# Kernel optimization log

Hardware: AMD Instinct MI355X
Metric: run time of the kernel (lower is better)

## Reference

```python
import jax, jax.numpy as jnp
import numpy as np

C = 16      # internal_channel
DG = 8      # deform groups
KK = 9      # 3x3 kernel


def conv2d(x, w, b, pad):
    out = jax.lax.conv_general_dilated(
        x, w, (1, 1), [(pad, pad), (pad, pad)],
        dimension_numbers=('NCHW', 'OIHW', 'NCHW'))
    return out + b[None, :, None, None]


def feature_extraction(img, w1, b1, w2, b2, w3, b3):
    f1 = jax.nn.relu(conv2d(img, w1, b1, 1))   # [B,C,H,W]
    f2 = jax.nn.relu(conv2d(f1, w2, b2, 0))    # [B,C,H-2,W-2]
    f3 = jax.nn.relu(conv2d(f2, w3, b3, 0))    # [B,C,H-4,W-4]
    return [f1, f2, f3]


def deform_conv(x, offset, w, b):
    # x: [B,C,H,W]; offset: [B, DG*KK*2, H, W] (y,x pairs); w: [Cout,C,3,3]
    B, Cin, H, W = x.shape
    Cg = Cin // DG
    off = offset.reshape(B, DG, KK, 2, H, W)
    ky = jnp.repeat(jnp.arange(3) - 1, 3)  # kernel y offsets (pad=1)
    kx = jnp.tile(jnp.arange(3) - 1, 3)
    base_y = jnp.arange(H).reshape(1, 1, 1, H, 1)
    base_x = jnp.arange(W).reshape(1, 1, 1, 1, W)
    sy = base_y + ky.reshape(1, 1, KK, 1, 1) + off[:, :, :, 0]  # [B,DG,KK,H,W]
    sx = base_x + kx.reshape(1, 1, KK, 1, 1) + off[:, :, :, 1]
    y0 = jnp.floor(sy)
    x0 = jnp.floor(sx)
    wy = (sy - y0)[:, :, None]  # [B,DG,1,KK,H,W]
    wx = (sx - x0)[:, :, None]
    y0i = y0.astype(jnp.int32)
    x0i = x0.astype(jnp.int32)
    xg = x.reshape(B, DG, Cg, H * W)

    def gather(yy, xx):
        valid = (yy >= 0) & (yy < H) & (xx >= 0) & (xx < W)  # zero pad outside
        idx = (jnp.clip(yy, 0, H - 1) * W + jnp.clip(xx, 0, W - 1))
        idx_b = jnp.broadcast_to(idx.reshape(B, DG, 1, KK, H * W), (B, DG, Cg, KK, H * W))
        src = jnp.broadcast_to(xg[:, :, :, None, :], (B, DG, Cg, KK, H * W))
        g = jnp.take_along_axis(src, idx_b, axis=-1).reshape(B, DG, Cg, KK, H, W)
        return g * valid[:, :, None].astype(x.dtype)

    v00 = gather(y0i, x0i)
    v01 = gather(y0i, x0i + 1)
    v10 = gather(y0i + 1, x0i)
    v11 = gather(y0i + 1, x0i + 1)
    s = (v00 * (1 - wy) * (1 - wx) + v01 * (1 - wy) * wx
         + v10 * wy * (1 - wx) + v11 * wy * wx)
    s = s.reshape(B, Cin, KK, H, W)
    out = jnp.einsum('bckhw,ock->bohw', s, w.reshape(w.shape[0], Cin, KK))
    return out + b[None, :, None, None]


def setup_inputs() -> dict:
    key = jax.random.key(0)
    ks = jax.random.split(key, 24)
    B, H, W = 4, 192, 192
    sc = 0.05
    d = {
        'ref_image': jax.random.normal(ks[0], (B, C, H, W), jnp.float32),
        'unreg_image': jax.random.normal(ks[1], (B, C, H, W), jnp.float32),
        'fe_w1': jax.random.normal(ks[2], (C, C, 3, 3), jnp.float32) * sc,
        'fe_b1': jnp.zeros((C,), jnp.float32),
        'fe_w2': jax.random.normal(ks[3], (C, C, 3, 3), jnp.float32) * sc,
        'fe_b2': jnp.zeros((C,), jnp.float32),
        'fe_w3': jax.random.normal(ks[4], (C, C, 3, 3), jnp.float32) * sc,
        'fe_b3': jnp.zeros((C,), jnp.float32),
        'off_w0': jax.random.normal(ks[5], (C, 2 * C, 3, 3), jnp.float32) * sc,
        'off_b0': jnp.zeros((C,), jnp.float32),
        'off_w1': jax.random.normal(ks[6], (C, 2 * C, 3, 3), jnp.float32) * sc,
        'off_b1': jnp.zeros((C,), jnp.float32),
        'off_w2': jax.random.normal(ks[7], (C, 2 * C, 3, 3), jnp.float32) * sc,
        'off_b2': jnp.zeros((C,), jnp.float32),
        'dcn_off_w': jax.random.normal(ks[8], (2 * DG * KK, C, 3, 3), jnp.float32) * sc,
        'dcn_off_b': jnp.zeros((2 * DG * KK,), jnp.float32),
        'dcn_w': jax.random.normal(ks[9], (C, C, 3, 3), jnp.float32) * sc,
        'dcn_b': jnp.zeros((C,), jnp.float32),
    }
    return d


def reference(ref_image, unreg_image, fe_w1, fe_b1, fe_w2, fe_b2, fe_w3, fe_b3,
              off_w0, off_b0, off_w1, off_b1, off_w2, off_b2,
              dcn_off_w, dcn_off_b, dcn_w, dcn_b):
    ref_f = feature_extraction(ref_image, fe_w1, fe_b1, fe_w2, fe_b2, fe_w3, fe_b3)
    unr_f = feature_extraction(unreg_image, fe_w1, fe_b1, fe_w2, fe_b2, fe_w3, fe_b3)
    off_ws = [(off_w0, off_b0), (off_w1, off_b1), (off_w2, off_b2)]
    aligned = [None, None, None]
    for i in range(2, -1, -1):  # coarse-to-fine as in the source loop
        cat = jnp.concatenate([ref_f[i], unr_f[i]], axis=1)        # [B,2C,h,w]
        off_feat = jax.nn.relu(conv2d(cat, off_ws[i][0], off_ws[i][1], 1))
        offsets = conv2d(off_feat, dcn_off_w, dcn_off_b, 1)        # [B,2*DG*KK,h,w]
        aligned[i] = deform_conv(unr_f[i], offsets, dcn_w, dcn_b)
    return tuple(aligned)
```

## Files before the change

kernel.cpp:

```cpp
#include <hip/hip_runtime.h>

typedef unsigned int uint;
typedef unsigned short ushort;
typedef __attribute__((ext_vector_type(8))) short bf16x8;
typedef __attribute__((ext_vector_type(4))) float f32x4;

__device__ inline ushort f2bf(float f) {
    uint u = __float_as_uint(f);
    u += 0x7fff + ((u >> 16) & 1);
    return (ushort)(u >> 16);
}
__device__ inline uint pkbf(float lo, float hi) {
    uint r;
    asm("v_cvt_pk_bf16_f32 %0, %1, %2" : "=v"(r) : "v"(lo), "v"(hi));
    return r;
}
__device__ inline float bflo(uint w) { return __uint_as_float(w << 16); }
__device__ inline float bfhi(uint w) { return __uint_as_float(w & 0xffff0000u); }

__global__ void packall_k(
    const float* __restrict__ fe_w1, const float* __restrict__ fe_w2,
    const float* __restrict__ fe_w3, const float* __restrict__ off_w0,
    const float* __restrict__ off_w1, const float* __restrict__ off_w2,
    const float* __restrict__ dcn_off_w, const float* __restrict__ dcn_w,
    ushort* __restrict__ pf1, ushort* __restrict__ pf2, ushort* __restrict__ pf3,
    ushort* __restrict__ po0, ushort* __restrict__ po1, ushort* __restrict__ po2,
    ushort* __restrict__ pow_, ushort* __restrict__ pd) {
    const int y = blockIdx.y;
    int i = blockIdx.x * 256 + threadIdx.x;
    const float* w; ushort* pk; int CIN, NT, KS;
    switch (y) {
        case 0: w = fe_w1;  pk = pf1;  CIN = 16; NT = 1; KS = 5; break;
        case 1: w = fe_w2;  pk = pf2;  CIN = 16; NT = 1; KS = 5; break;
        case 2: w = fe_w3;  pk = pf3;  CIN = 16; NT = 1; KS = 5; break;
        case 3: w = off_w0; pk = po0;  CIN = 32; NT = 1; KS = 9; break;
        case 4: w = off_w1; pk = po1;  CIN = 32; NT = 1; KS = 9; break;
        case 5: w = off_w2; pk = po2;  CIN = 32; NT = 1; KS = 9; break;
        case 6: w = dcn_off_w; pk = pow_; CIN = 16; NT = 9; KS = 5; break;
        default: w = dcn_w; pk = pd;   CIN = 16; NT = 1; KS = 5; break;
    }
    if (i >= KS * NT * 512) return;
    int e = i & 7, lane = (i >> 3) & 63, rest = i >> 9;
    int nt = rest % NT, ks = rest / NT;
    int k = ks * 32 + (lane >> 4) * 8 + e;
    int n = nt * 16 + (lane & 15);
    int t, ci;
    if (CIN == 16) { t = k >> 4; ci = k & 15; } else { t = k >> 5; ci = k & 31; }
    float v = (t < 9) ? w[(n * CIN + ci) * 9 + t] : 0.f;
    pk[i] = f2bf(v);
}

template <bool PLANAR>
__launch_bounds__(256)
__global__ void fe_mfma_k(const float* __restrict__ pA, const float* __restrict__ pB,
                          const ushort* __restrict__ catin,
                          const ushort* __restrict__ pack, const float* __restrict__ bias,
                          ushort* __restrict__ catout,
                          int H, int W, int OH, int OW, int pad) {
    __shared__ ushort patch[324 * 16];
    const int tid = threadIdx.x;
    const int tx0 = blockIdx.x * 16, ty0 = blockIdx.y * 16;
    const int b = blockIdx.z & 3, img = blockIdx.z >> 2;
    const int bx = tx0 - pad, by = ty0 - pad;
    const int HW = H * W;

    if (PLANAR) {
        const float* inb = (img ? pB : pA) + (size_t)(b * 16) * HW;
        for (int pos = tid; pos < 324; pos += 256) {
            int r = pos / 18, c = pos - r * 18;
            int gy = by + r, gx = bx + c;
            bool ok = (unsigned)gy < (unsigned)H && (unsigned)gx < (unsigned)W;
            int base = gy * W + gx;
            uint o16[8];
#pragma unroll
            for (int ii = 0; ii < 8; ++ii) {
                float lo = ok ? inb[(2 * ii) * HW + base] : 0.f;
                float hi = ok ? inb[(2 * ii + 1) * HW + base] : 0.f;
                o16[ii] = (uint)f2bf(lo) | ((uint)f2bf(hi) << 16);
            }
            *(uint4*)(patch + pos * 16) = *(uint4*)&o16[0];
            *(uint4*)(patch + pos * 16 + 8) = *(uint4*)&o16[4];
        }
    } else {
        for (int c = tid; c < 648; c += 256) {
            int pos = c >> 1, h = c & 1;
            int r = pos / 18, col = pos - r * 18;
            int gy = by + r, gx = bx + col;
            uint4 v = make_uint4(0, 0, 0, 0);
            if ((unsigned)gy < (unsigned)H && (unsigned)gx < (unsigned)W)
                v = *(const uint4*)(catin + ((size_t)(b * H + gy) * W + gx) * 32 + img * 16 + h * 8);
            *(uint4*)(patch + pos * 16 + h * 8) = v;
        }
    }
    __syncthreads();

    const int lane = tid & 63, wv = tid >> 6;
    const int g = lane >> 4, ci0 = (g & 1) * 8, rowx = lane & 15;
    f32x4 acc[4];
    float bv = bias[rowx];
#pragma unroll
    for (int m = 0; m < 4; ++m) acc[m] = f32x4{bv, bv, bv, bv};

#pragma unroll
    for (int ks = 0; ks < 5; ++ks) {
        int t = 2 * ks + (g >> 1);
        int dy = t < 9 ? t / 3 : 0;
        int dx = t < 9 ? t - (t / 3) * 3 : 0;
        bf16x8 a[4];
#pragma unroll
        for (int m = 0; m < 4; ++m) {
            int r = wv * 4 + m + dy, cc = rowx + dx;
            a[m] = *(const bf16x8*)(patch + (r * 18 + cc) * 16 + ci0);
        }
        bf16x8 bfrag = *(const bf16x8*)((const uint4*)pack + ks * 64 + lane);
#pragma unroll
        for (int m = 0; m < 4; ++m)
            acc[m] = __builtin_amdgcn_mfma_f32_16x16x32_bf16(a[m], bfrag, acc[m], 0, 0, 0);
    }

    const int oxb = g * 4;
#pragma unroll
    for (int m = 0; m < 4; ++m) {
        int gy = ty0 + wv * 4 + m;
        if (gy >= OH) continue;
#pragma unroll
        for (int j = 0; j < 4; ++j) {
            int gx = tx0 + oxb + j;
            if (gx < OW)
                catout[((size_t)(b * OH + gy) * OW + gx) * 32 + img * 16 + rowx] =
                    f2bf(fmaxf(acc[m][j], 0.f));
        }
    }
}

__launch_bounds__(256)
__global__ void off_mfma_k(const ushort* __restrict__ c0, const ushort* __restrict__ c1,
                           const ushort* __restrict__ c2,
                           const ushort* __restrict__ pk0, const ushort* __restrict__ pk1,
                           const ushort* __restrict__ pk2,
                           const float* __restrict__ b0, const float* __restrict__ b1,
                           const float* __restrict__ b2,
                           ushort* __restrict__ f0, ushort* __restrict__ f1,
                           ushort* __restrict__ f2) {
    const int z = blockIdx.z, s = z >> 2, b = z & 3;
    const int H = 192 - 2 * s, W = H;
    const ushort* cat  = s == 0 ? c0 : (s == 1 ? c1 : c2);
    const ushort* pack = s == 0 ? pk0 : (s == 1 ? pk1 : pk2);
    const float* bias  = s == 0 ? b0 : (s == 1 ? b1 : b2);
    ushort* out        = s == 0 ? f0 : (s == 1 ? f1 : f2);

    __shared__ ushort patch[324 * 32];
    const int tid = threadIdx.x;
    const int tx0 = blockIdx.x * 16, ty0 = blockIdx.y * 16;
    const int bx = tx0 - 1, by = ty0 - 1;

    for (int c = tid; c < 1296; c += 256) {
        int pos = c >> 2, h = c & 3;
        int r = pos / 18, col = pos - r * 18;
        int gy = by + r, gx = bx + col;
        uint4 v = make_uint4(0, 0, 0, 0);
        if ((unsigned)gy < (unsigned)H && (unsigned)gx < (unsigned)W)
            v = *(const uint4*)(cat + ((size_t)(b * H + gy) * W + gx) * 32 + h * 8);
        *(uint4*)(patch + pos * 32 + h * 8) = v;
    }
    __syncthreads();

    const int lane = tid & 63, wv = tid >> 6;
    const int g = lane >> 4, ci0 = g * 8, rowx = lane & 15;
    f32x4 acc[4];
    float bv = bias[rowx];
#pragma unroll
    for (int m = 0; m < 4; ++m) acc[m] = f32x4{bv, bv, bv, bv};

#pragma unroll
    for (int ks = 0; ks < 9; ++ks) {
        int dy = ks / 3, dx = ks - (ks / 3) * 3;
        bf16x8 a[4];
#pragma unroll
        for (int m = 0; m < 4; ++m) {
            int r = wv * 4 + m + dy, cc = rowx + dx;
            a[m] = *(const bf16x8*)(patch + (r * 18 + cc) * 32 + ci0);
        }
        bf16x8 bfrag = *(const bf16x8*)((const uint4*)pack + ks * 64 + lane);
#pragma unroll
        for (int m = 0; m < 4; ++m)
            acc[m] = __builtin_amdgcn_mfma_f32_16x16x32_bf16(a[m], bfrag, acc[m], 0, 0, 0);
    }

    const int oxb = g * 4;
#pragma unroll
    for (int m = 0; m < 4; ++m) {
        int gy = ty0 + wv * 4 + m;
        if (gy >= H) continue;
#pragma unroll
        for (int j = 0; j < 4; ++j) {
            int gx = tx0 + oxb + j;
            if (gx < W)
                out[((size_t)(b * H + gy) * W + gx) * 16 + rowx] = f2bf(fmaxf(acc[m][j], 0.f));
        }
    }
}

__launch_bounds__(256)
__global__ void dcn_fused_k(const ushort* __restrict__ c0, const ushort* __restrict__ c1,
                            const ushort* __restrict__ c2,
                            const ushort* __restrict__ fb0, const ushort* __restrict__ fb1,
                            const ushort* __restrict__ fb2,
                            const ushort* __restrict__ owPack, const float* __restrict__ ob,
                            const ushort* __restrict__ pd, const float* __restrict__ db,
                            float* __restrict__ o0, float* __restrict__ o1,
                            float* __restrict__ o2) {
    const int z = blockIdx.z;
    const int s = z >> 2, b = z & 3;
    const int H = 192 - 2 * s, W = H;
    const ushort* cat = s == 0 ? c0 : (s == 1 ? c1 : c2);
    const ushort* fb  = s == 0 ? fb0 : (s == 1 ? fb1 : fb2);
    float* out        = s == 0 ? o0 : (s == 1 ? o1 : o2);
    const int HW = H * W;
    const size_t pixb = (size_t)b * HW;

    __shared__ uint   xtu[8 * 484];
    __shared__ ushort ot[4 * 16 * 152];

    const int tid = threadIdx.x;
    const int tx0 = blockIdx.x * 16, ty0 = blockIdx.y * 16;

    {
        const int bx3 = tx0 - 3, by3 = ty0 - 3;
        for (int pos = tid; pos < 484; pos += 256) {
            int r = pos / 22, c = pos - r * 22;
            int gy2 = by3 + r, gx2 = bx3 + c;
            uint4 va = make_uint4(0, 0, 0, 0), vb = va;
            if ((unsigned)gy2 < (unsigned)H && (unsigned)gx2 < (unsigned)W) {
                const ushort* src = cat + (pixb + gy2 * W + gx2) * 32 + 16;
                va = *(const uint4*)src;
                vb = *(const uint4*)(src + 8);
            }
            xtu[0 * 484 + pos] = va.x; xtu[1 * 484 + pos] = va.y;
            xtu[2 * 484 + pos] = va.z; xtu[3 * 484 + pos] = va.w;
            xtu[4 * 484 + pos] = vb.x; xtu[5 * 484 + pos] = vb.y;
            xtu[6 * 484 + pos] = vb.z; xtu[7 * 484 + pos] = vb.w;
        }
    }
    __syncthreads();

    const int lane = tid & 63, wv = tid >> 6;
    const int g = lane >> 4, rowx = lane & 15, half = g & 1;
    const int ci0 = half * 8;
    const int px = tx0 + rowx;
    const float bv2 = db[rowx];
    ushort* otw = ot + wv * (16 * 152);

#pragma unroll 1
    for (int m = 0; m < 4; ++m) {
        const int py = ty0 + wv * 4 + m;

        auto loadA = [&](int ks) -> uint4 {
            int t = 2 * ks + (g >> 1);
            int tc = t < 9 ? t : 0;
            int dy = tc / 3, dx = tc - (tc / 3) * 3;
            int gya = ty0 - 1 + wv * 4 + m + dy;
            int gxa = tx0 - 1 + rowx + dx;
            uint4 r = make_uint4(0, 0, 0, 0);
            if ((unsigned)gya < (unsigned)H && (unsigned)gxa < (unsigned)W)
                r = *(const uint4*)(fb + ((size_t)(b * H + gya) * W + gxa) * 16 + ci0);
            return r;
        };

        f32x4 acc[9];
#pragma unroll
        for (int n = 0; n < 9; ++n) {
            float bv = ob[n * 16 + rowx];
            acc[n] = f32x4{bv, bv, bv, bv};
        }
        uint4 avc = loadA(0);
#pragma unroll 1
        for (int ks = 0; ks < 5; ++ks) {
            uint4 avn = make_uint4(0, 0, 0, 0);
            if (ks < 4) avn = loadA(ks + 1);
            bf16x8 a = *(bf16x8*)&avc;
            const uint4* bp = (const uint4*)owPack + (size_t)(ks * 9) * 64 + lane;
#pragma unroll
            for (int n = 0; n < 9; ++n) {
                bf16x8 bfrag = *(const bf16x8*)(bp + (size_t)n * 64);
                acc[n] = __builtin_amdgcn_mfma_f32_16x16x32_bf16(a, bfrag, acc[n], 0, 0, 0);
            }
            avc = avn;
        }

#pragma unroll
        for (int n = 0; n < 9; ++n) {
            int ch = n * 16 + rowx;
            int dg = ch / 18;
            int rem = ch - dg * 18;
            int col = (rem >> 1) * 16 + dg * 2 + (rem & 1);
            uint p01 = pkbf(acc[n][0], acc[n][1]);
            uint p23 = pkbf(acc[n][2], acc[n][3]);
            otw[(g * 4 + 0) * 152 + col] = (ushort)p01;
            otw[(g * 4 + 1) * 152 + col] = (ushort)(p01 >> 16);
            otw[(g * 4 + 2) * 152 + col] = (ushort)p23;
            otw[(g * 4 + 3) * 152 + col] = (ushort)(p23 >> 16);
        }

        auto loadOV = [&](int ks) -> uint4 {
            int t = 2 * ks + (g >> 1);
            uint4 r = make_uint4(0, 0, 0, 0);
            if (t < 9) r = *(const uint4*)(otw + rowx * 152 + t * 16 + half * 8);
            return r;
        };

        f32x4 acc2 = f32x4{bv2, bv2, bv2, bv2};
        uint4 ovc = loadOV(0);
#pragma unroll 1
        for (int ks = 0; ks < 5; ++ks) {
            uint4 ovn = make_uint4(0, 0, 0, 0);
            if (ks < 4) ovn = loadOV(ks + 1);
            const int t = 2 * ks + (g >> 1);
            const bool tv = (t < 9);
            const int t3 = t / 3;
            const int ky = (tv ? t3 : 0) - 1, kx = (tv ? t - t3 * 3 : 0) - 1;

            uint a2[4];
            if (tv) {
                uint ovv[4] = {ovc.x, ovc.y, ovc.z, ovc.w};
#pragma unroll
                for (int d = 0; d < 4; ++d) {
                    const int dgA = half * 4 + d;
                    uint u = ovv[d];
                    float sy = (float)(py + ky) + bflo(u);
                    float sx = (float)(px + kx) + bfhi(u);
                    float fy = floorf(sy), fx = floorf(sx);
                    int y0 = (int)fy, x0 = (int)fx;
                    float wy = sy - fy, wx = sx - fx;
                    float wy1 = 1.f - wy, wx1 = 1.f - wx;
                    float w00 = wy1 * wx1, w01 = wy1 * wx, w10 = wy * wx1, w11 = wy * wx;
                    int ly = y0 - (ty0 - 3), lx = x0 - (tx0 - 3);
                    float2 v00, v01, v10, v11;
                    if ((unsigned)ly <= 20u && (unsigned)lx <= 20u) {
                        const uint* tt = &xtu[dgA * 484 + ly * 22 + lx];
                        uint u00 = tt[0], u01 = tt[1], u10 = tt[22], u11 = tt[23];
                        v00 = make_float2(bflo(u00), bfhi(u00));
                        v01 = make_float2(bflo(u01), bfhi(u01));
                        v10 = make_float2(bflo(u10), bfhi(u10));
                        v11 = make_float2(bflo(u11), bfhi(u11));
                    } else {
                        v00 = v01 = v10 = v11 = make_float2(0.f, 0.f);
                        bool y0v = (unsigned)y0 < (unsigned)H;
                        bool y1v = (unsigned)(y0 + 1) < (unsigned)H;
                        bool x0v = (unsigned)x0 < (unsigned)W;
                        bool x1v = (unsigned)(x0 + 1) < (unsigned)W;
                        const ushort* cg = cat + ((size_t)pixb + (size_t)y0 * W + x0) * 32 + 16 + 2 * dgA;
                        if (y0v && x0v) { uint uu = *(const uint*)cg;                 v00 = make_float2(bflo(uu), bfhi(uu)); }
                        if (y0v && x1v) { uint uu = *(const uint*)(cg + 32);          v01 = make_float2(bflo(uu), bfhi(uu)); }
                        if (y1v && x0v) { uint uu = *(const uint*)(cg + 32 * W);      v10 = make_float2(bflo(uu), bfhi(uu)); }
                        if (y1v && x1v) { uint uu = *(const uint*)(cg + 32 * W + 32); v11 = make_float2(bflo(uu), bfhi(uu)); }
                    }
                    float s0 = w00 * v00.x + w01 * v01.x + w10 * v10.x + w11 * v11.x;
                    float s1 = w00 * v00.y + w01 * v01.y + w10 * v10.y + w11 * v11.y;
                    a2[d] = pkbf(s0, s1);
                }
            } else {
                a2[0] = a2[1] = a2[2] = a2[3] = 0u;
            }
            uint4 av = make_uint4(a2[0], a2[1], a2[2], a2[3]);
            bf16x8 af = *(bf16x8*)&av;
            bf16x8 dfrag = *(const bf16x8*)((const uint4*)pd + ks * 64 + lane);
            acc2 = __builtin_amdgcn_mfma_f32_16x16x32_bf16(af, dfrag, acc2, 0, 0, 0);
            ovc = ovn;
        }

        if (py < H) {
            float* op = out + (size_t)(b * 16 + rowx) * HW + (size_t)py * W;
#pragma unroll
            for (int j = 0; j < 4; ++j) {
                int gx2 = tx0 + g * 4 + j;
                if (gx2 < W) op[gx2] = acc2[j];
            }
        }
    }
}

extern "C" void kernel_launch(void* const* d_in, const int* in_sizes, int n_in,
                              void* d_out, int out_size, void* d_ws, size_t ws_size,
                              hipStream_t stream) {
    const float* ref_image = (const float*)d_in[0];
    const float* unreg_image = (const float*)d_in[1];
    const float* fe_w1 = (const float*)d_in[2];
    const float* fe_b1 = (const float*)d_in[3];
    const float* fe_w2 = (const float*)d_in[4];
    const float* fe_b2 = (const float*)d_in[5];
    const float* fe_w3 = (const float*)d_in[6];
    const float* fe_b3 = (const float*)d_in[7];
    const float* off_w0 = (const float*)d_in[8];
    const float* off_b0 = (const float*)d_in[9];
    const float* off_w1 = (const float*)d_in[10];
    const float* off_b1 = (const float*)d_in[11];
    const float* off_w2 = (const float*)d_in[12];
    const float* off_b2 = (const float*)d_in[13];
    const float* dcn_off_w = (const float*)d_in[14];
    const float* dcn_off_b = (const float*)d_in[15];
    const float* dcn_w = (const float*)d_in[16];
    const float* dcn_b = (const float*)d_in[17];

    const size_t pix[3] = {4ul * 192 * 192, 4ul * 190 * 190, 4ul * 188 * 188};
    const size_t szf[3] = {pix[0] * 16, pix[1] * 16, pix[2] * 16};

    size_t o = 0;
    auto take = [&](size_t bytes) {
        void* r = (char*)d_ws + o;
        o += (bytes + 255) & ~(size_t)255;
        return r;
    };
    ushort* cat[3]; ushort* fb[3];
    ushort* pf[3]; ushort* po[3]; ushort* owPack; ushort* pd;
    for (int s = 0; s < 3; ++s) cat[s] = (ushort*)take(pix[s] * 32 * 2);
    for (int s = 0; s < 3; ++s) fb[s] = (ushort*)take(pix[s] * 16 * 2);
    for (int s = 0; s < 3; ++s) pf[s] = (ushort*)take(2560 * 2);
    for (int s = 0; s < 3; ++s) po[s] = (ushort*)take(4608 * 2);
    owPack = (ushort*)take(23040 * 2);
    pd = (ushort*)take(2560 * 2);

    float* out0 = (float*)d_out;
    float* out1 = out0 + szf[0];
    float* out2 = out1 + szf[1];

    dim3 blk(256);

    packall_k<<<dim3(90, 8), blk, 0, stream>>>(
        fe_w1, fe_w2, fe_w3, off_w0, off_w1, off_w2, dcn_off_w, dcn_w,
        pf[0], pf[1], pf[2], po[0], po[1], po[2], owPack, pd);

    fe_mfma_k<true><<<dim3(12, 12, 8), blk, 0, stream>>>(
        ref_image, unreg_image, nullptr, pf[0], fe_b1, cat[0], 192, 192, 192, 192, 1);
    fe_mfma_k<false><<<dim3(12, 12, 8), blk, 0, stream>>>(
        nullptr, nullptr, cat[0], pf[1], fe_b2, cat[1], 192, 192, 190, 190, 0);
    fe_mfma_k<false><<<dim3(12, 12, 8), blk, 0, stream>>>(
        nullptr, nullptr, cat[1], pf[2], fe_b3, cat[2], 190, 190, 188, 188, 0);

    off_mfma_k<<<dim3(12, 12, 12), blk, 0, stream>>>(
        cat[0], cat[1], cat[2], po[0], po[1], po[2],
        off_b0, off_b1, off_b2, fb[0], fb[1], fb[2]);

    dcn_fused_k<<<dim3(12, 12, 12), blk, 0, stream>>>(
        cat[0], cat[1], cat[2], fb[0], fb[1], fb[2],
        owPack, dcn_off_b, pd, dcn_b, out0, out1, out2);
}
```

Before: 174.4 us.

## Software-pipeline next row's offset-conv loads across the deformable sampling stage

The offset-conv operand loads and MFMA stage for row m+1 are moved so they overlap the bilinear sampling stage of row m. All five A fragments for the next row are issued before the sampling loop, and the next row's offset MFMAs and LDS repack run after the current row's output store. The first row is computed in a prologue. This hides global-load latency behind ALU and LDS work, at the cost of about 20 extra VGPRs for the prefetched operands. A small hoist also precomputes the float base coordinates per kernel tap.

```diff
diff --git a/kernel.cpp b/kernel.cpp
--- a/kernel.cpp
+++ b/kernel.cpp
@@ -251,43 +251,39 @@
     const float bv2 = db[rowx];
     ushort* otw = ot + wv * (16 * 152);
 
-#pragma unroll 1
-    for (int m = 0; m < 4; ++m) {
-        const int py = ty0 + wv * 4 + m;
-
-        auto loadA = [&](int ks) -> uint4 {
-            int t = 2 * ks + (g >> 1);
-            int tc = t < 9 ? t : 0;
-            int dy = tc / 3, dx = tc - (tc / 3) * 3;
-            int gya = ty0 - 1 + wv * 4 + m + dy;
-            int gxa = tx0 - 1 + rowx + dx;
-            uint4 r = make_uint4(0, 0, 0, 0);
-            if ((unsigned)gya < (unsigned)H && (unsigned)gxa < (unsigned)W)
-                r = *(const uint4*)(fb + ((size_t)(b * H + gya) * W + gxa) * 16 + ci0);
-            return r;
-        };
-
-        f32x4 acc[9];
+    auto loadA = [&](int ks, int mrow) -> uint4 {
+        int t = 2 * ks + (g >> 1);
+        int tc = t < 9 ? t : 0;
+        int dy = tc / 3, dx = tc - (tc / 3) * 3;
+        int gya = ty0 - 1 + wv * 4 + mrow + dy;
+        int gxa = tx0 - 1 + rowx + dx;
+        uint4 r = make_uint4(0, 0, 0, 0);
+        if ((unsigned)gya < (unsigned)H && (unsigned)gxa < (unsigned)W)
+            r = *(const uint4*)(fb + ((size_t)(b * H + gya) * W + gxa) * 16 + ci0);
+        return r;
+    };
+
+    auto mfma45 = [&](uint4 a0, uint4 a1, uint4 a2c, uint4 a3, uint4 a4,
+                      f32x4 (&acc)[9]) {
 #pragma unroll
         for (int n = 0; n < 9; ++n) {
             float bv = ob[n * 16 + rowx];
             acc[n] = f32x4{bv, bv, bv, bv};
         }
-        uint4 avc = loadA(0);
 #pragma unroll 1
         for (int ks = 0; ks < 5; ++ks) {
-            uint4 avn = make_uint4(0, 0, 0, 0);
-            if (ks < 4) avn = loadA(ks + 1);
-            bf16x8 a = *(bf16x8*)&avc;
+            uint4 avv = ks == 0 ? a0 : ks == 1 ? a1 : ks == 2 ? a2c : ks == 3 ? a3 : a4;
+            bf16x8 a = *(bf16x8*)&avv;
             const uint4* bp = (const uint4*)owPack + (size_t)(ks * 9) * 64 + lane;
 #pragma unroll
             for (int n = 0; n < 9; ++n) {
                 bf16x8 bfrag = *(const bf16x8*)(bp + (size_t)n * 64);
                 acc[n] = __builtin_amdgcn_mfma_f32_16x16x32_bf16(a, bfrag, acc[n], 0, 0, 0);
             }
-            avc = avn;
-        }
-
+        }
+    };
+
+    auto repack = [&](f32x4 (&acc)[9]) {
 #pragma unroll
         for (int n = 0; n < 9; ++n) {
             int ch = n * 16 + rowx;
@@ -301,6 +297,26 @@
             otw[(g * 4 + 2) * 152 + col] = (ushort)p23;
             otw[(g * 4 + 3) * 152 + col] = (ushort)(p23 >> 16);
         }
+    };
+
+    {
+        uint4 a0 = loadA(0, 0), a1 = loadA(1, 0), a2c = loadA(2, 0),
+              a3 = loadA(3, 0), a4 = loadA(4, 0);
+        f32x4 acc[9];
+        mfma45(a0, a1, a2c, a3, a4, acc);
+        repack(acc);
+    }
+
+#pragma unroll 1
+    for (int m = 0; m < 4; ++m) {
+        const int py = ty0 + wv * 4 + m;
+        const int mn = m + 1;
+
+        uint4 na0, na1, na2, na3, na4;
+        if (mn < 4) {
+            na0 = loadA(0, mn); na1 = loadA(1, mn); na2 = loadA(2, mn);
+            na3 = loadA(3, mn); na4 = loadA(4, mn);
+        }
 
         auto loadOV = [&](int ks) -> uint4 {
             int t = 2 * ks + (g >> 1);
@@ -318,7 +334,8 @@
             const int t = 2 * ks + (g >> 1);
             const bool tv = (t < 9);
             const int t3 = t / 3;
-            const int ky = (tv ? t3 : 0) - 1, kx = (tv ? t - t3 * 3 : 0) - 1;
+            const float pyk = (float)(py + (tv ? t3 : 0) - 1);
+            const float pxk = (float)(px + (tv ? t - t3 * 3 : 0) - 1);
 
             uint a2[4];
             if (tv) {
@@ -327,8 +344,8 @@
                 for (int d = 0; d < 4; ++d) {
                     const int dgA = half * 4 + d;
                     uint u = ovv[d];
-                    float sy = (float)(py + ky) + bflo(u);
-                    float sx = (float)(px + kx) + bfhi(u);
+                    float sy = pyk + bflo(u);
+                    float sx = pxk + bfhi(u);
                     float fy = floorf(sy), fx = floorf(sx);
                     int y0 = (int)fy, x0 = (int)fx;
                     float wy = sy - fy, wx = sx - fx;
@@ -349,7 +366,7 @@
                         bool y1v = (unsigned)(y0 + 1) < (unsigned)H;
                         bool x0v = (unsigned)x0 < (unsigned)W;
                         bool x1v = (unsigned)(x0 + 1) < (unsigned)W;
-                        const ushort* cg = cat + ((size_t)pixb + (size_t)y0 * W + x0) * 32 + 16 + 2 * dgA;
+                        const ushort* cg = cat + (pixb + (size_t)y0 * W + x0) * 32 + 16 + 2 * dgA;
                         if (y0v && x0v) { uint uu = *(const uint*)cg;                 v00 = make_float2(bflo(uu), bfhi(uu)); }
                         if (y0v && x1v) { uint uu = *(const uint*)(cg + 32);          v01 = make_float2(bflo(uu), bfhi(uu)); }
                         if (y1v && x0v) { uint uu = *(const uint*)(cg + 32 * W);      v10 = make_float2(bflo(uu), bfhi(uu)); }
@@ -376,6 +393,12 @@
                 int gx2 = tx0 + g * 4 + j;
                 if (gx2 < W) op[gx2] = acc2[j];
             }
+        }
+
+        if (mn < 4) {
+            f32x4 acc[9];
+            mfma45(na0, na1, na2, na3, na4, acc);
+            repack(acc);
         }
     }
 }
```

Result: slower. 198.9 us (+14.0%).
